# Kernel tuning notes

Hardware: AMD Instinct MI355X
Metric: run time of the kernel (lower is better)

## Reference

```python
import jax, jax.numpy as jnp
import numpy as np

N_NODES = 50000
N_EDGES = 400000
NUM_FEATS = 128
LATENT_DIM_Y = 64
HIDDEN = 512
OUT = 2


def gcn_conv(x, edge_index, W, b, num_nodes):
    """PyG GCNConv: add self-loops, symmetric normalization, x @ W then scatter-add."""
    x = x @ W  # [N, out_ch]
    loop = jnp.arange(num_nodes)
    row = jnp.concatenate([edge_index[0], loop])  # source nodes
    col = jnp.concatenate([edge_index[1], loop])  # target nodes
    deg = jax.ops.segment_sum(jnp.ones_like(col, dtype=x.dtype), col, num_segments=num_nodes)
    dinv = jnp.where(deg > 0, jax.lax.rsqrt(deg), 0.0)
    norm = dinv[row] * dinv[col]  # [E+N]
    msgs = norm[:, None] * x[row]  # gather source features, scale
    out = jax.ops.segment_sum(msgs, col, num_segments=num_nodes)
    return out + b


def setup_inputs() -> dict:
    key = jax.random.key(0)
    k1, k2, k3, k4, k5, k6, k7 = jax.random.split(key, 7)
    in_ch = NUM_FEATS + LATENT_DIM_Y
    inputs = {
        "edge_index": jax.random.randint(k1, (2, N_EDGES), 0, N_NODES),
        "X": jax.random.normal(k2, (N_NODES, NUM_FEATS), dtype=jnp.float32),
        "u_Y": jax.random.normal(k3, (N_NODES, LATENT_DIM_Y), dtype=jnp.float32),
        "W1": jax.random.normal(k4, (in_ch, HIDDEN), dtype=jnp.float32) / np.sqrt(in_ch),
        "b1": jnp.zeros((HIDDEN,), dtype=jnp.float32),
        "W2": jax.random.normal(k5, (HIDDEN, OUT), dtype=jnp.float32) / np.sqrt(HIDDEN),
        "b2": jnp.zeros((OUT,), dtype=jnp.float32),
    }
    return inputs


def reference(edge_index, X, u_Y, W1, b1, W2, b2):
    latent = jnp.concatenate([u_Y, X], axis=1)  # [N, latent+feats]
    h = jax.nn.relu(gcn_conv(latent, edge_index, W1, b1, N_NODES))
    y = gcn_conv(h, edge_index, W2, b2, N_NODES)
    # nn.Softmax() on a 2D tensor defaults to dim=1
    return jax.nn.softmax(y, axis=1)
```

## Files before the change

kernel.cpp:

```cpp
#include <hip/hip_runtime.h>

#define N_NODES 50000
#define N_EDGES 400000
#define FEATS   128
#define LAT     64
#define IN_CH   192
#define HID     512
#define MB      64
#define NB      196

#define CNT_BLKS 1563
#define CVT_BLKS 9375
#define W1_BLKS  384

typedef __attribute__((ext_vector_type(8))) short bf16x8;
typedef __attribute__((ext_vector_type(4))) float f32x4;

static inline int cdiv(int a, int b) { return (a + b - 1) / b; }

__device__ __forceinline__ unsigned short f2bf(float f) {
    unsigned int u = __float_as_uint(f);
    u = (u + 0x7fffu + ((u >> 16) & 1u)) >> 16;
    return (unsigned short)u;
}
__device__ __forceinline__ float bf_lo(unsigned int u) {
    return __uint_as_float(u << 16);
}
__device__ __forceinline__ float bf_hi(unsigned int u) {
    return __uint_as_float(u & 0xffff0000u);
}

__global__ __launch_bounds__(256) void
k_front(const int* __restrict__ col, int* __restrict__ cnt,
        const float* __restrict__ uY, const float* __restrict__ X,
        unsigned short* __restrict__ latent,
        const float* __restrict__ W1, unsigned short* __restrict__ W1f) {
    int bid = blockIdx.x;
    if (bid < CNT_BLKS) {
        int e = bid * 256 + threadIdx.x;
        if (e < N_EDGES) atomicAdd(&cnt[col[e]], 1);
    } else if (bid < CNT_BLKS + CVT_BLKS) {
        int idx = (bid - CNT_BLKS) * 256 + threadIdx.x;
        int i = idx / 48, q = idx % 48;
        const float4* uY4 = (const float4*)uY;
        const float4* X4  = (const float4*)X;
        float4 v = (q < LAT / 4) ? uY4[i * (LAT / 4) + q]
                                 : X4[i * (FEATS / 4) + (q - LAT / 4)];
        uint2 o;
        o.x = (unsigned int)f2bf(v.x) | ((unsigned int)f2bf(v.y) << 16);
        o.y = (unsigned int)f2bf(v.z) | ((unsigned int)f2bf(v.w) << 16);
        ((uint2*)latent)[idx] = o;
    } else {
        int idx = (bid - CNT_BLKS - CVT_BLKS) * 256 + threadIdx.x;
        if (idx < IN_CH * HID) {
            int k = idx / HID, n = idx % HID;
            int ntile = n >> 4, nn = n & 15;
            int kc = k >> 5, q = (k >> 3) & 3, j = k & 7;
            int dst = (((ntile * 6 + kc) * 64 + q * 16 + nn) << 3) + j;
            W1f[dst] = f2bf(W1[idx]);
        }
    }
}

__global__ __launch_bounds__(256) void
k_block_reduce(const int* __restrict__ cnt, int* __restrict__ bsum) {
    __shared__ int wsums[4];
    int i = blockIdx.x * 256 + threadIdx.x;
    int v = (i < N_NODES) ? cnt[i] : 0;
#pragma unroll
    for (int off = 32; off; off >>= 1) v += __shfl_down(v, off);
    if ((threadIdx.x & 63) == 0) wsums[threadIdx.x >> 6] = v;
    __syncthreads();
    if (threadIdx.x == 0) bsum[blockIdx.x] = wsums[0] + wsums[1] + wsums[2] + wsums[3];
}

__global__ __launch_bounds__(256) void
k_scan_bsums(const int* __restrict__ bsum, int* __restrict__ bex) {
    __shared__ int wsums[4];
    int t = threadIdx.x, lane = t & 63, wid = t >> 6;
    int v = (t < NB) ? bsum[t] : 0;
    int x = v;
#pragma unroll
    for (int off = 1; off < 64; off <<= 1) {
        int y = __shfl_up(x, off);
        if (lane >= off) x += y;
    }
    if (lane == 63) wsums[wid] = x;
    __syncthreads();
    int wo = 0;
    for (int w = 0; w < wid; ++w) wo += wsums[w];
    if (t < NB) bex[t] = wo + x - v;
}

__global__ __launch_bounds__(256) void
k_block_scan(const int* __restrict__ cnt, const int* __restrict__ bex,
             int* __restrict__ row_start, int* __restrict__ cursor,
             float* __restrict__ dinv) {
    __shared__ int wsums[4];
    int t = threadIdx.x, lane = t & 63, wid = t >> 6;
    int i = blockIdx.x * 256 + t;
    int v = (i < N_NODES) ? cnt[i] : 0;
    int x = v;
#pragma unroll
    for (int off = 1; off < 64; off <<= 1) {
        int y = __shfl_up(x, off);
        if (lane >= off) x += y;
    }
    if (lane == 63) wsums[wid] = x;
    __syncthreads();
    int wo = 0;
    for (int w = 0; w < wid; ++w) wo += wsums[w];
    int ex = bex[blockIdx.x] + wo + x - v;
    if (i < N_NODES) {
        row_start[i] = ex;
        cursor[i]    = ex;
        dinv[i]      = rsqrtf((float)(v + 1));
    }
    if (blockIdx.x == 0 && t == 0) row_start[N_NODES] = N_EDGES;
}

__global__ void k_scatter(const int* __restrict__ ei, int* __restrict__ cursor,
                          int* __restrict__ csr_src) {
    int e = blockIdx.x * blockDim.x + threadIdx.x;
    if (e >= N_EDGES) return;
    int r = ei[e];
    int c = ei[N_EDGES + e];
    int pos = atomicAdd(&cursor[c], 1);
    csr_src[pos] = r;
}

__global__ __launch_bounds__(256) void
k_gather_agg(const int* __restrict__ row_start, const int* __restrict__ csr_src,
             const float* __restrict__ dinv,
             const unsigned short* __restrict__ latent, unsigned short* __restrict__ agg) {
    int w    = blockIdx.x * 4 + (threadIdx.x >> 6);
    int lane = threadIdx.x & 63;
    if (w >= N_NODES) return;
    int qt = lane >> 4, l = lane & 15;
    int c0 = l * 6;
    const unsigned int* __restrict__ L = (const unsigned int*)latent;

    float di = dinv[w];
    float acc[12];
    if (qt == 0) {
        const unsigned int* p = L + w * 96 + c0;
#pragma unroll
        for (int d = 0; d < 6; ++d) {
            unsigned int u = p[d];
            acc[2 * d]     = di * bf_lo(u);
            acc[2 * d + 1] = di * bf_hi(u);
        }
    } else {
#pragma unroll
        for (int d = 0; d < 12; ++d) acc[d] = 0.f;
    }

    int jlo = row_start[w], jhi = row_start[w + 1];
    int j = jlo + qt;
    int r = (j < jhi) ? csr_src[j] : 0;
    for (; j < jhi; j += 4) {
        int rn = (j + 4 < jhi) ? csr_src[j + 4] : 0;
        float wt = dinv[r];
        const unsigned int* p = L + r * 96 + c0;
        unsigned int u0 = p[0], u1 = p[1], u2 = p[2], u3 = p[3], u4 = p[4], u5 = p[5];
        acc[0]  = fmaf(wt, bf_lo(u0), acc[0]);
        acc[1]  = fmaf(wt, bf_hi(u0), acc[1]);
        acc[2]  = fmaf(wt, bf_lo(u1), acc[2]);
        acc[3]  = fmaf(wt, bf_hi(u1), acc[3]);
        acc[4]  = fmaf(wt, bf_lo(u2), acc[4]);
        acc[5]  = fmaf(wt, bf_hi(u2), acc[5]);
        acc[6]  = fmaf(wt, bf_lo(u3), acc[6]);
        acc[7]  = fmaf(wt, bf_hi(u3), acc[7]);
        acc[8]  = fmaf(wt, bf_lo(u4), acc[8]);
        acc[9]  = fmaf(wt, bf_hi(u4), acc[9]);
        acc[10] = fmaf(wt, bf_lo(u5), acc[10]);
        acc[11] = fmaf(wt, bf_hi(u5), acc[11]);
        r = rn;
    }

#pragma unroll
    for (int d = 0; d < 12; ++d) {
        acc[d] += __shfl_xor(acc[d], 16);
        acc[d] += __shfl_xor(acc[d], 32);
    }

    if (qt == 0) {
        unsigned int* qp = (unsigned int*)agg + w * 96 + c0;
#pragma unroll
        for (int d = 0; d < 6; ++d)
            qp[d] = (unsigned int)f2bf(di * acc[2 * d]) |
                    ((unsigned int)f2bf(di * acc[2 * d + 1]) << 16);
    }
}

__global__ __launch_bounds__(256, 2) void
k_gemm_mfma(const unsigned short* __restrict__ agg, const unsigned short* __restrict__ W1f,
            const float* __restrict__ b1, const float* __restrict__ W2,
            float* __restrict__ y_pre) {
    __shared__ unsigned short Af[MB * IN_CH];
    __shared__ float red[4][MB][2];

    int t  = threadIdx.x;
    int m0 = blockIdx.x * MB;

    {
        const uint4* src = (const uint4*)agg;
        for (int idx = t; idx < MB * 24; idx += 256) {
            int row = idx / 24, c = idx % 24;
            int g = m0 + row;
            uint4 v = make_uint4(0u, 0u, 0u, 0u);
            if (g < N_NODES) v = src[(size_t)g * 24 + c];
            int mt = row >> 4, m = row & 15, kc = c >> 2, q = c & 3;
            ((uint4*)Af)[(mt * 6 + kc) * 64 + q * 16 + m] = v;
        }
    }
    __syncthreads();

    int wid = t >> 6, lane = t & 63;
    int nl = lane & 15, q = lane >> 4;

    float b1v[8], w2a[8], w2b[8];
#pragma unroll
    for (int nt = 0; nt < 8; ++nt) {
        int n = wid * 128 + nt * 16 + nl;
        b1v[nt] = b1[n];
        w2a[nt] = W2[n * 2 + 0];
        w2b[nt] = W2[n * 2 + 1];
    }

    f32x4 acc[4][8];
#pragma unroll
    for (int mt = 0; mt < 4; ++mt)
#pragma unroll
        for (int nt = 0; nt < 8; ++nt) acc[mt][nt] = (f32x4){0.f, 0.f, 0.f, 0.f};

    const bf16x8* Afv = (const bf16x8*)Af;
    const bf16x8* Bv  = (const bf16x8*)W1f;
#pragma unroll
    for (int kc = 0; kc < 6; ++kc) {
        bf16x8 a[4];
#pragma unroll
        for (int mt = 0; mt < 4; ++mt) a[mt] = Afv[(mt * 6 + kc) * 64 + lane];
#pragma unroll
        for (int nt = 0; nt < 8; ++nt) {
            bf16x8 b = Bv[((wid * 8 + nt) * 6 + kc) * 64 + lane];
#pragma unroll
            for (int mt = 0; mt < 4; ++mt)
                acc[mt][nt] = __builtin_amdgcn_mfma_f32_16x16x32_bf16(a[mt], b, acc[mt][nt], 0, 0, 0);
        }
    }

#pragma unroll
    for (int mt = 0; mt < 4; ++mt) {
#pragma unroll
        for (int r = 0; r < 4; ++r) {
            float p0 = 0.f, p1 = 0.f;
#pragma unroll
            for (int nt = 0; nt < 8; ++nt) {
                float h = fmaxf(acc[mt][nt][r] + b1v[nt], 0.f);
                p0 = fmaf(h, w2a[nt], p0);
                p1 = fmaf(h, w2b[nt], p1);
            }
#pragma unroll
            for (int off = 1; off < 16; off <<= 1) {
                p0 += __shfl_xor(p0, off);
                p1 += __shfl_xor(p1, off);
            }
            if (nl == 0) {
                int row = mt * 16 + q * 4 + r;
                red[wid][row][0] = p0;
                red[wid][row][1] = p1;
            }
        }
    }
    __syncthreads();
    if (t < MB * 2) {
        int row = t >> 1, j = t & 1;
        float s = red[0][row][j] + red[1][row][j] + red[2][row][j] + red[3][row][j];
        int g = m0 + row;
        if (g < N_NODES) y_pre[g * 2 + j] = s;
    }
}

__global__ __launch_bounds__(256) void
k_gather_y(const int* __restrict__ row_start, const int* __restrict__ csr_src,
           const float* __restrict__ dinv,
           const float* __restrict__ y_pre, const float* __restrict__ b2,
           float* __restrict__ out) {
    int i  = blockIdx.x * 32 + (threadIdx.x >> 3);
    int l8 = threadIdx.x & 7;
    if (i >= N_NODES) return;
    float di = dinv[i];
    float a0 = 0.f, a1 = 0.f;
    if (l8 == 0) {
        a0 = di * y_pre[i * 2 + 0];
        a1 = di * y_pre[i * 2 + 1];
    }
    int jlo = row_start[i], jhi = row_start[i + 1];
    for (int j = jlo + l8; j < jhi; j += 8) {
        int   r  = csr_src[j];
        float wt = dinv[r];
        a0 = fmaf(wt, y_pre[r * 2 + 0], a0);
        a1 = fmaf(wt, y_pre[r * 2 + 1], a1);
    }
#pragma unroll
    for (int off = 1; off < 8; off <<= 1) {
        a0 += __shfl_xor(a0, off);
        a1 += __shfl_xor(a1, off);
    }
    if (l8 == 0) {
        float ya = di * a0 + b2[0];
        float yb = di * a1 + b2[1];
        float mx = fmaxf(ya, yb);
        float e0 = expf(ya - mx);
        float e1 = expf(yb - mx);
        float inv = 1.0f / (e0 + e1);
        out[i * 2 + 0] = e0 * inv;
        out[i * 2 + 1] = e1 * inv;
    }
}


extern "C" void kernel_launch(void* const* d_in, const int* in_sizes, int n_in,
                              void* d_out, int out_size, void* d_ws, size_t ws_size,
                              hipStream_t stream) {
    const int*   ei = (const int*)d_in[0];
    const float* X  = (const float*)d_in[1];
    const float* uY = (const float*)d_in[2];
    const float* W1 = (const float*)d_in[3];
    const float* b1 = (const float*)d_in[4];
    const float* W2 = (const float*)d_in[5];
    const float* b2 = (const float*)d_in[6];
    float* out = (float*)d_out;

    char* ws = (char*)d_ws;
    auto carve = [&](size_t bytes) {
        char* p = ws;
        ws += (bytes + 255) & ~size_t(255);
        return p;
    };
    int*   cnt       = (int*)carve(N_NODES * sizeof(int));
    int*   bsum      = (int*)carve(NB * sizeof(int));
    int*   bex       = (int*)carve(NB * sizeof(int));
    int*   row_start = (int*)carve((N_NODES + 1) * sizeof(int));
    int*   cursor    = (int*)carve(N_NODES * sizeof(int));
    int*   csr_src   = (int*)carve((size_t)N_EDGES * sizeof(int));
    float* dinv      = (float*)carve(N_NODES * sizeof(float));
    unsigned short* latent = (unsigned short*)carve((size_t)N_NODES * IN_CH * 2);
    unsigned short* aggb   = (unsigned short*)carve((size_t)N_NODES * IN_CH * 2);
    unsigned short* W1f    = (unsigned short*)carve((size_t)IN_CH * HID * 2);
    float* y_pre     = (float*)carve((size_t)N_NODES * 2 * sizeof(float));

    hipMemsetAsync(cnt, 0, N_NODES * sizeof(int), stream);
    k_front       <<<CNT_BLKS + CVT_BLKS + W1_BLKS, 256, 0, stream>>>(
                        ei + N_EDGES, cnt, uY, X, latent, W1, W1f);
    k_block_reduce<<<NB, 256, 0, stream>>>(cnt, bsum);
    k_scan_bsums  <<<1, 256, 0, stream>>>(bsum, bex);
    k_block_scan  <<<NB, 256, 0, stream>>>(cnt, bex, row_start, cursor, dinv);
    k_scatter     <<<cdiv(N_EDGES, 256), 256, 0, stream>>>(ei, cursor, csr_src);

    k_gather_agg  <<<cdiv(N_NODES, 4), 256, 0, stream>>>(row_start, csr_src, dinv, latent, aggb);

    k_gemm_mfma   <<<cdiv(N_NODES, MB), 256, 0, stream>>>(aggb, W1f, b1, W2, y_pre);

    k_gather_y    <<<cdiv(N_NODES, 32), 256, 0, stream>>>(row_start, csr_src, dinv, y_pre, b2, out);
}
```

Measured before the change: 202.5 us.

## Fuse neighbor aggregation into MFMA GEMM and collapse CSR scan to one kernel

The gather-aggregate kernel is merged into the GEMM kernel. Each block aggregates its 32 rows straight into shared memory in MFMA layout, so the bf16 agg buffer no longer makes a global round trip. The three-kernel prefix scan is replaced by one kernel in which each block takes its base offset with an atomicAdd on a global counter. Row ends are now computed as start+cnt, because block order makes the offsets a non-ordered but valid partition. MB is halved to 32 so the grid has more blocks and occupancy is higher, at the cost of reloading W1 more often per row and doing less GEMM work per wave.

```diff
diff --git a/kernel.cpp b/kernel.cpp
--- a/kernel.cpp
+++ b/kernel.cpp
@@ -6,7 +6,7 @@
 #define LAT     64
 #define IN_CH   192
 #define HID     512
-#define MB      64
+#define MB      32
 #define NB      196
 
 #define CNT_BLKS 1563
@@ -63,22 +63,14 @@
 }
 
 __global__ __launch_bounds__(256) void
-k_block_reduce(const int* __restrict__ cnt, int* __restrict__ bsum) {
+k_csr_scan(const int* __restrict__ cnt, int* __restrict__ gctr,
+           int* __restrict__ row_start, int* __restrict__ cursor,
+           float* __restrict__ dinv) {
     __shared__ int wsums[4];
-    int i = blockIdx.x * 256 + threadIdx.x;
+    __shared__ int sbase;
+    int t = threadIdx.x, lane = t & 63, wid = t >> 6;
+    int i = blockIdx.x * 256 + t;
     int v = (i < N_NODES) ? cnt[i] : 0;
-#pragma unroll
-    for (int off = 32; off; off >>= 1) v += __shfl_down(v, off);
-    if ((threadIdx.x & 63) == 0) wsums[threadIdx.x >> 6] = v;
-    __syncthreads();
-    if (threadIdx.x == 0) bsum[blockIdx.x] = wsums[0] + wsums[1] + wsums[2] + wsums[3];
-}
-
-__global__ __launch_bounds__(256) void
-k_scan_bsums(const int* __restrict__ bsum, int* __restrict__ bex) {
-    __shared__ int wsums[4];
-    int t = threadIdx.x, lane = t & 63, wid = t >> 6;
-    int v = (t < NB) ? bsum[t] : 0;
     int x = v;
 #pragma unroll
     for (int off = 1; off < 64; off <<= 1) {
@@ -89,34 +81,17 @@
     __syncthreads();
     int wo = 0;
     for (int w = 0; w < wid; ++w) wo += wsums[w];
-    if (t < NB) bex[t] = wo + x - v;
-}
-
-__global__ __launch_bounds__(256) void
-k_block_scan(const int* __restrict__ cnt, const int* __restrict__ bex,
-             int* __restrict__ row_start, int* __restrict__ cursor,
-             float* __restrict__ dinv) {
-    __shared__ int wsums[4];
-    int t = threadIdx.x, lane = t & 63, wid = t >> 6;
-    int i = blockIdx.x * 256 + t;
-    int v = (i < N_NODES) ? cnt[i] : 0;
-    int x = v;
-#pragma unroll
-    for (int off = 1; off < 64; off <<= 1) {
-        int y = __shfl_up(x, off);
-        if (lane >= off) x += y;
-    }
-    if (lane == 63) wsums[wid] = x;
+    if (t == 0) {
+        int tot = wsums[0] + wsums[1] + wsums[2] + wsums[3];
+        sbase = atomicAdd(gctr, tot);
+    }
     __syncthreads();
-    int wo = 0;
-    for (int w = 0; w < wid; ++w) wo += wsums[w];
-    int ex = bex[blockIdx.x] + wo + x - v;
+    int ex = sbase + wo + x - v;
     if (i < N_NODES) {
         row_start[i] = ex;
         cursor[i]    = ex;
         dinv[i]      = rsqrtf((float)(v + 1));
     }
-    if (blockIdx.x == 0 && t == 0) row_start[N_NODES] = N_EDGES;
 }
 
 __global__ void k_scatter(const int* __restrict__ ei, int* __restrict__ cursor,
@@ -129,135 +104,125 @@
     csr_src[pos] = r;
 }
 
-__global__ __launch_bounds__(256) void
-k_gather_agg(const int* __restrict__ row_start, const int* __restrict__ csr_src,
-             const float* __restrict__ dinv,
-             const unsigned short* __restrict__ latent, unsigned short* __restrict__ agg) {
-    int w    = blockIdx.x * 4 + (threadIdx.x >> 6);
-    int lane = threadIdx.x & 63;
-    if (w >= N_NODES) return;
+__global__ __launch_bounds__(256, 3) void
+k_gather_gemm(const int* __restrict__ row_start, const int* __restrict__ cnt,
+              const int* __restrict__ csr_src, const float* __restrict__ dinv,
+              const unsigned short* __restrict__ latent,
+              const unsigned short* __restrict__ W1f,
+              const float* __restrict__ b1, const float* __restrict__ W2,
+              float* __restrict__ y_pre) {
+    __shared__ unsigned short Af[MB * IN_CH];
+    __shared__ float red[4][MB][2];
+
+    int t = threadIdx.x;
+    int wave = t >> 6, lane = t & 63;
+    int m0 = blockIdx.x * MB;
     int qt = lane >> 4, l = lane & 15;
     int c0 = l * 6;
     const unsigned int* __restrict__ L = (const unsigned int*)latent;
 
-    float di = dinv[w];
-    float acc[12];
-    if (qt == 0) {
-        const unsigned int* p = L + w * 96 + c0;
-#pragma unroll
-        for (int d = 0; d < 6; ++d) {
-            unsigned int u = p[d];
-            acc[2 * d]     = di * bf_lo(u);
-            acc[2 * d + 1] = di * bf_hi(u);
-        }
-    } else {
+    for (int mi = 0; mi < 8; ++mi) {
+        int m = wave * 8 + mi;
+        int g = m0 + m;
+        float acc[12];
 #pragma unroll
         for (int d = 0; d < 12; ++d) acc[d] = 0.f;
-    }
-
-    int jlo = row_start[w], jhi = row_start[w + 1];
-    int j = jlo + qt;
-    int r = (j < jhi) ? csr_src[j] : 0;
-    for (; j < jhi; j += 4) {
-        int rn = (j + 4 < jhi) ? csr_src[j + 4] : 0;
-        float wt = dinv[r];
-        const unsigned int* p = L + r * 96 + c0;
-        unsigned int u0 = p[0], u1 = p[1], u2 = p[2], u3 = p[3], u4 = p[4], u5 = p[5];
-        acc[0]  = fmaf(wt, bf_lo(u0), acc[0]);
-        acc[1]  = fmaf(wt, bf_hi(u0), acc[1]);
-        acc[2]  = fmaf(wt, bf_lo(u1), acc[2]);
-        acc[3]  = fmaf(wt, bf_hi(u1), acc[3]);
-        acc[4]  = fmaf(wt, bf_lo(u2), acc[4]);
-        acc[5]  = fmaf(wt, bf_hi(u2), acc[5]);
-        acc[6]  = fmaf(wt, bf_lo(u3), acc[6]);
-        acc[7]  = fmaf(wt, bf_hi(u3), acc[7]);
-        acc[8]  = fmaf(wt, bf_lo(u4), acc[8]);
-        acc[9]  = fmaf(wt, bf_hi(u4), acc[9]);
-        acc[10] = fmaf(wt, bf_lo(u5), acc[10]);
-        acc[11] = fmaf(wt, bf_hi(u5), acc[11]);
-        r = rn;
-    }
-
-#pragma unroll
-    for (int d = 0; d < 12; ++d) {
-        acc[d] += __shfl_xor(acc[d], 16);
-        acc[d] += __shfl_xor(acc[d], 32);
-    }
-
-    if (qt == 0) {
-        unsigned int* qp = (unsigned int*)agg + w * 96 + c0;
-#pragma unroll
-        for (int d = 0; d < 6; ++d)
-            qp[d] = (unsigned int)f2bf(di * acc[2 * d]) |
-                    ((unsigned int)f2bf(di * acc[2 * d + 1]) << 16);
-    }
-}
-
-__global__ __launch_bounds__(256, 2) void
-k_gemm_mfma(const unsigned short* __restrict__ agg, const unsigned short* __restrict__ W1f,
-            const float* __restrict__ b1, const float* __restrict__ W2,
-            float* __restrict__ y_pre) {
-    __shared__ unsigned short Af[MB * IN_CH];
-    __shared__ float red[4][MB][2];
-
-    int t  = threadIdx.x;
-    int m0 = blockIdx.x * MB;
-
-    {
-        const uint4* src = (const uint4*)agg;
-        for (int idx = t; idx < MB * 24; idx += 256) {
-            int row = idx / 24, c = idx % 24;
-            int g = m0 + row;
-            uint4 v = make_uint4(0u, 0u, 0u, 0u);
-            if (g < N_NODES) v = src[(size_t)g * 24 + c];
-            int mt = row >> 4, m = row & 15, kc = c >> 2, q = c & 3;
-            ((uint4*)Af)[(mt * 6 + kc) * 64 + q * 16 + m] = v;
+        float di = 0.f;
+        if (g < N_NODES) {
+            di = dinv[g];
+            if (qt == 0) {
+                const unsigned int* p = L + g * 96 + c0;
+#pragma unroll
+                for (int d = 0; d < 6; ++d) {
+                    unsigned int u = p[d];
+                    acc[2 * d]     = di * bf_lo(u);
+                    acc[2 * d + 1] = di * bf_hi(u);
+                }
+            }
+            int jlo = row_start[g];
+            int jhi = jlo + cnt[g];
+            int j = jlo + qt;
+            int r = (j < jhi) ? csr_src[j] : 0;
+            for (; j < jhi; j += 4) {
+                int rn = (j + 4 < jhi) ? csr_src[j + 4] : 0;
+                float wt = dinv[r];
+                const unsigned int* p = L + r * 96 + c0;
+                unsigned int u0 = p[0], u1 = p[1], u2 = p[2], u3 = p[3], u4 = p[4], u5 = p[5];
+                acc[0]  = fmaf(wt, bf_lo(u0), acc[0]);
+                acc[1]  = fmaf(wt, bf_hi(u0), acc[1]);
+                acc[2]  = fmaf(wt, bf_lo(u1), acc[2]);
+                acc[3]  = fmaf(wt, bf_hi(u1), acc[3]);
+                acc[4]  = fmaf(wt, bf_lo(u2), acc[4]);
+                acc[5]  = fmaf(wt, bf_hi(u2), acc[5]);
+                acc[6]  = fmaf(wt, bf_lo(u3), acc[6]);
+                acc[7]  = fmaf(wt, bf_hi(u3), acc[7]);
+                acc[8]  = fmaf(wt, bf_lo(u4), acc[8]);
+                acc[9]  = fmaf(wt, bf_hi(u4), acc[9]);
+                acc[10] = fmaf(wt, bf_lo(u5), acc[10]);
+                acc[11] = fmaf(wt, bf_hi(u5), acc[11]);
+                r = rn;
+            }
+        }
+#pragma unroll
+        for (int d = 0; d < 12; ++d) {
+            acc[d] += __shfl_xor(acc[d], 16);
+            acc[d] += __shfl_xor(acc[d], 32);
+        }
+        if (qt == 0) {
+            int mt = m >> 4, ml = m & 15;
+#pragma unroll
+            for (int dd = 0; dd < 6; ++dd) {
+                int d = c0 + dd;
+                unsigned int val = (unsigned int)f2bf(di * acc[2 * dd]) |
+                                   ((unsigned int)f2bf(di * acc[2 * dd + 1]) << 16);
+                int dw = ((mt * 6 + (d >> 4)) * 64 + ((d >> 2) & 3) * 16 + ml) * 4 + (d & 3);
+                ((unsigned int*)Af)[dw] = val;
+            }
         }
     }
     __syncthreads();
 
-    int wid = t >> 6, lane = t & 63;
     int nl = lane & 15, q = lane >> 4;
 
     float b1v[8], w2a[8], w2b[8];
 #pragma unroll
     for (int nt = 0; nt < 8; ++nt) {
-        int n = wid * 128 + nt * 16 + nl;
+        int n = wave * 128 + nt * 16 + nl;
         b1v[nt] = b1[n];
         w2a[nt] = W2[n * 2 + 0];
         w2b[nt] = W2[n * 2 + 1];
     }
 
-    f32x4 acc[4][8];
-#pragma unroll
-    for (int mt = 0; mt < 4; ++mt)
-#pragma unroll
-        for (int nt = 0; nt < 8; ++nt) acc[mt][nt] = (f32x4){0.f, 0.f, 0.f, 0.f};
+    f32x4 acc2[2][8];
+#pragma unroll
+    for (int mt = 0; mt < 2; ++mt)
+#pragma unroll
+        for (int nt = 0; nt < 8; ++nt) acc2[mt][nt] = (f32x4){0.f, 0.f, 0.f, 0.f};
 
     const bf16x8* Afv = (const bf16x8*)Af;
     const bf16x8* Bv  = (const bf16x8*)W1f;
 #pragma unroll
     for (int kc = 0; kc < 6; ++kc) {
-        bf16x8 a[4];
-#pragma unroll
-        for (int mt = 0; mt < 4; ++mt) a[mt] = Afv[(mt * 6 + kc) * 64 + lane];
+        bf16x8 a[2];
+#pragma unroll
+        for (int mt = 0; mt < 2; ++mt) a[mt] = Afv[(mt * 6 + kc) * 64 + lane];
 #pragma unroll
         for (int nt = 0; nt < 8; ++nt) {
-            bf16x8 b = Bv[((wid * 8 + nt) * 6 + kc) * 64 + lane];
-#pragma unroll
-            for (int mt = 0; mt < 4; ++mt)
-                acc[mt][nt] = __builtin_amdgcn_mfma_f32_16x16x32_bf16(a[mt], b, acc[mt][nt], 0, 0, 0);
-        }
-    }
-
-#pragma unroll
-    for (int mt = 0; mt < 4; ++mt) {
+            bf16x8 b = Bv[((wave * 8 + nt) * 6 + kc) * 64 + lane];
+#pragma unroll
+            for (int mt = 0; mt < 2; ++mt)
+                acc2[mt][nt] = __builtin_amdgcn_mfma_f32_16x16x32_bf16(a[mt], b, acc2[mt][nt], 0, 0, 0);
+        }
+    }
+
+#pragma unroll
+    for (int mt = 0; mt < 2; ++mt) {
 #pragma unroll
         for (int r = 0; r < 4; ++r) {
             float p0 = 0.f, p1 = 0.f;
 #pragma unroll
             for (int nt = 0; nt < 8; ++nt) {
-                float h = fmaxf(acc[mt][nt][r] + b1v[nt], 0.f);
+                float h = fmaxf(acc2[mt][nt][r] + b1v[nt], 0.f);
                 p0 = fmaf(h, w2a[nt], p0);
                 p1 = fmaf(h, w2b[nt], p1);
             }
@@ -268,8 +233,8 @@
             }
             if (nl == 0) {
                 int row = mt * 16 + q * 4 + r;
-                red[wid][row][0] = p0;
-                red[wid][row][1] = p1;
+                red[wave][row][0] = p0;
+                red[wave][row][1] = p1;
             }
         }
     }
@@ -283,8 +248,8 @@
 }
 
 __global__ __launch_bounds__(256) void
-k_gather_y(const int* __restrict__ row_start, const int* __restrict__ csr_src,
-           const float* __restrict__ dinv,
+k_gather_y(const int* __restrict__ row_start, const int* __restrict__ cnt,
+           const int* __restrict__ csr_src, const float* __restrict__ dinv,
            const float* __restrict__ y_pre, const float* __restrict__ b2,
            float* __restrict__ out) {
     int i  = blockIdx.x * 32 + (threadIdx.x >> 3);
@@ -296,7 +261,7 @@
         a0 = di * y_pre[i * 2 + 0];
         a1 = di * y_pre[i * 2 + 1];
     }
-    int jlo = row_start[i], jhi = row_start[i + 1];
+    int jlo = row_start[i], jhi = jlo + cnt[i];
     for (int j = jlo + l8; j < jhi; j += 8) {
         int   r  = csr_src[j];
         float wt = dinv[r];
@@ -339,29 +304,25 @@
         ws += (bytes + 255) & ~size_t(255);
         return p;
     };
+    int*   gctr      = (int*)carve(sizeof(int));
     int*   cnt       = (int*)carve(N_NODES * sizeof(int));
-    int*   bsum      = (int*)carve(NB * sizeof(int));
-    int*   bex       = (int*)carve(NB * sizeof(int));
-    int*   row_start = (int*)carve((N_NODES + 1) * sizeof(int));
+    int*   row_start = (int*)carve(N_NODES * sizeof(int));
     int*   cursor    = (int*)carve(N_NODES * sizeof(int));
     int*   csr_src   = (int*)carve((size_t)N_EDGES * sizeof(int));
     float* dinv      = (float*)carve(N_NODES * sizeof(float));
     unsigned short* latent = (unsigned short*)carve((size_t)N_NODES * IN_CH * 2);
-    unsigned short* aggb   = (unsigned short*)carve((size_t)N_NODES * IN_CH * 2);
     unsigned short* W1f    = (unsigned short*)carve((size_t)IN_CH * HID * 2);
     float* y_pre     = (float*)carve((size_t)N_NODES * 2 * sizeof(float));
 
-    hipMemsetAsync(cnt, 0, N_NODES * sizeof(int), stream);
-    k_front       <<<CNT_BLKS + CVT_BLKS + W1_BLKS, 256, 0, stream>>>(
-                        ei + N_EDGES, cnt, uY, X, latent, W1, W1f);
-    k_block_reduce<<<NB, 256, 0, stream>>>(cnt, bsum);
-    k_scan_bsums  <<<1, 256, 0, stream>>>(bsum, bex);
-    k_block_scan  <<<NB, 256, 0, stream>>>(cnt, bex, row_start, cursor, dinv);
-    k_scatter     <<<cdiv(N_EDGES, 256), 256, 0, stream>>>(ei, cursor, csr_src);
-
-    k_gather_agg  <<<cdiv(N_NODES, 4), 256, 0, stream>>>(row_start, csr_src, dinv, latent, aggb);
-
-    k_gemm_mfma   <<<cdiv(N_NODES, MB), 256, 0, stream>>>(aggb, W1f, b1, W2, y_pre);
-
-    k_gather_y    <<<cdiv(N_NODES, 32), 256, 0, stream>>>(row_start, csr_src, dinv, y_pre, b2, out);
-}
+    hipMemsetAsync(gctr, 0, 256 + N_NODES * sizeof(int), stream);
+
+    k_front     <<<CNT_BLKS + CVT_BLKS + W1_BLKS, 256, 0, stream>>>(
+                      ei + N_EDGES, cnt, uY, X, latent, W1, W1f);
+    k_csr_scan  <<<NB, 256, 0, stream>>>(cnt, gctr, row_start, cursor, dinv);
+    k_scatter   <<<cdiv(N_EDGES, 256), 256, 0, stream>>>(ei, cursor, csr_src);
+
+    k_gather_gemm<<<cdiv(N_NODES, MB), 256, 0, stream>>>(
+                      row_start, cnt, csr_src, dinv, latent, W1f, b1, W2, y_pre);
+
+    k_gather_y  <<<cdiv(N_NODES, 32), 256, 0, stream>>>(row_start, cnt, csr_src, dinv, y_pre, b2, out);
+}
```

Result: slower. 206.9 us (+2.2%).
